# Kernel tuning notes

Hardware: AMD Instinct MI355X
Metric: run time of the kernel (lower is better)

Reference implementation:

```python
import jax, jax.numpy as jnp
import numpy as np

EPS = 1e-8
NEG_INF = -9e15  # matches torch masked_fill value


def setup_inputs() -> dict:
    key = jax.random.key(0)
    k1, k2 = jax.random.split(key)
    B, D = 4096, 512
    p1 = jax.random.normal(k1, (B, D), dtype=jnp.float32)
    p2 = jax.random.normal(k2, (B, D), dtype=jnp.float32)
    return {"p1": p1, "p2": p2}


def reference(p1, p2):
    # NT-Xent / InfoNCE loss as in SimCLR_MODEL.contrastive_loss (temperature = 1).
    z = jnp.concatenate([p1, p2], axis=0)              # [N, D], N = 2B
    # cosine similarity == GEMM of L2-normalized rows (torch eps clamp = 1e-8)
    zn = z / jnp.maximum(jnp.linalg.norm(z, axis=-1, keepdims=True), EPS)
    sim = zn @ zn.T                                     # [N, N]
    N = sim.shape[0]
    idx = jnp.arange(N)
    sim = sim.at[idx, idx].set(NEG_INF)                 # mask self-similarity
    # positive pair of row i is row (i + N/2) mod N (eye rolled by N/2)
    pos = sim[idx, (idx + N // 2) % N]                  # [N]
    nll = -pos + jax.nn.logsumexp(sim, axis=-1)
    return jnp.mean(nll)
```

## Files before the change

### kernel.cpp

```cpp
#include <hip/hip_runtime.h>
#include <hip/hip_bf16.h>
#include <math.h>

#define N_TOT 8192
#define HALF_N 4096
#define D_DIM 512
#define BM 256
#define BK 64
#define NKIT (D_DIM / BK)
#define NTILES 528
#define THREADS 512

typedef float f32x4_t __attribute__((ext_vector_type(4)));
typedef long long i64x2 __attribute__((ext_vector_type(2)));

typedef __attribute__((address_space(1))) unsigned int g_u32;
typedef __attribute__((address_space(3))) unsigned int l_u32;

__global__ __launch_bounds__(256) void k_normalize(
    const float* __restrict__ p1, const float* __restrict__ p2,
    unsigned char* __restrict__ zf8, float* __restrict__ rowsum,
    float* __restrict__ out)
{
    const int w = threadIdx.x >> 6;
    const int lane = threadIdx.x & 63;
    const int row = blockIdx.x * 4 + w;

    if (threadIdx.x < 4) rowsum[blockIdx.x * 4 + threadIdx.x] = 0.0f;
    if (blockIdx.x == 0 && threadIdx.x == 0) out[0] = 0.0f;

    const float* src = (row < HALF_N) ? p1 + (size_t)row * D_DIM
                                      : p2 + (size_t)(row - HALF_N) * D_DIM;
    float4 a = *(const float4*)(src + lane * 4);
    float4 b = *(const float4*)(src + 256 + lane * 4);
    float s = a.x*a.x + a.y*a.y + a.z*a.z + a.w*a.w
            + b.x*b.x + b.y*b.y + b.z*b.z + b.w*b.w;
    #pragma unroll
    for (int m = 1; m < 64; m <<= 1) s += __shfl_xor(s, m, 64);
    float inv = 1.0f / fmaxf(sqrtf(s), 1e-8f);

    int pk0 = __builtin_amdgcn_cvt_pk_fp8_f32(a.x * inv, a.y * inv, 0, false);
    pk0     = __builtin_amdgcn_cvt_pk_fp8_f32(a.z * inv, a.w * inv, pk0, true);
    int pk1 = __builtin_amdgcn_cvt_pk_fp8_f32(b.x * inv, b.y * inv, 0, false);
    pk1     = __builtin_amdgcn_cvt_pk_fp8_f32(b.z * inv, b.w * inv, pk1, true);

    unsigned char* dst = zf8 + (size_t)row * D_DIM;
    const int o0 = lane * 4;
    const int o1 = 256 + lane * 4;
    const int d0 = (o0 & ~63) + ((o0 >> 3) & 3) * 16 + ((o0 >> 5) & 1) * 8 + (o0 & 4);
    const int d1 = (o1 & ~63) + ((o1 >> 3) & 3) * 16 + ((o1 >> 5) & 1) * 8 + (o1 & 4);
    *(int*)(dst + d0) = pk0;
    *(int*)(dst + d1) = pk1;
}

__global__ __launch_bounds__(THREADS, 2) void k_gemm(
    const unsigned char* __restrict__ zf8,
    float* __restrict__ rowsum, float* __restrict__ pos)
{
    __shared__ __align__(16) unsigned char As[2][BM * BK];
    __shared__ __align__(16) unsigned char Bs[2][BM * BK];

    const int tid = threadIdx.x;
    const int lane = tid & 63;
    const int w = tid >> 6;
    const int wr = w >> 2, wc = w & 3;
    const int q = lane >> 4, l15 = lane & 15;

    const int t0 = blockIdx.x;
    const int t = (t0 & 7) * (NTILES / 8) + (t0 >> 3);

    int bi = (int)((sqrtf(8.0f * (float)t + 1.0f) - 1.0f) * 0.5f);
    while ((bi + 1) * (bi + 2) / 2 <= t) ++bi;
    while (bi * (bi + 1) / 2 > t) --bi;
    const int bx = bi;
    const int by = t - bi * (bi + 1) / 2;
    const bool isDiag = (bx == by);
    const bool hasPos = (bx - by == (HALF_N / BM));
    const int rowBase = by * BM;
    const int colBase = bx * BM;

    const int ci0 = tid;
    const int ci1 = tid + THREADS;
    const int r0 = ci0 >> 2, cc0 = ci0 & 3;
    const int r1 = ci1 >> 2, cc1 = ci1 & 3;
    const int gc0 = cc0 ^ ((r0 >> 1) & 3);
    const int gc1 = cc1 ^ ((r1 >> 1) & 3);

    const unsigned char* gA0 = zf8 + (size_t)(rowBase + r0) * D_DIM + gc0 * 16;
    const unsigned char* gA1 = zf8 + (size_t)(rowBase + r1) * D_DIM + gc1 * 16;
    const unsigned char* gB0 = zf8 + (size_t)(colBase + r0) * D_DIM + gc0 * 16;
    const unsigned char* gB1 = zf8 + (size_t)(colBase + r1) * D_DIM + gc1 * 16;

    auto stage = [&](int buf, int kblk) {
        const int kb = kblk * BK;
        __builtin_amdgcn_global_load_lds((const g_u32*)(gA0 + kb), (l_u32*)&As[buf][ci0 * 16], 16, 0, 0);
        __builtin_amdgcn_global_load_lds((const g_u32*)(gA1 + kb), (l_u32*)&As[buf][ci1 * 16], 16, 0, 0);
        __builtin_amdgcn_global_load_lds((const g_u32*)(gB0 + kb), (l_u32*)&Bs[buf][ci0 * 16], 16, 0, 0);
        __builtin_amdgcn_global_load_lds((const g_u32*)(gB1 + kb), (l_u32*)&Bs[buf][ci1 * 16], 16, 0, 0);
    };

    f32x4_t acc[8][4] = {};

    stage(0, 0);

    #pragma unroll
    for (int it = 0; it < NKIT; it++) {
        const int cur = it & 1;
        __syncthreads();
        if (it + 1 < NKIT) stage(cur ^ 1, it + 1);

        i64x2 aF[8], bF[4];
        #pragma unroll
        for (int i = 0; i < 8; i++) {
            const int ra = wr * 128 + i * 16 + l15;
            aF[i] = *(const i64x2*)&As[cur][ra * BK + (q ^ ((ra >> 1) & 3)) * 16];
        }
        #pragma unroll
        for (int j = 0; j < 4; j++) {
            const int rb = wc * 64 + j * 16 + l15;
            bF[j] = *(const i64x2*)&Bs[cur][rb * BK + (q ^ ((rb >> 1) & 3)) * 16];
        }
        #pragma unroll
        for (int h = 0; h < 2; h++)
            #pragma unroll
            for (int i = 0; i < 8; i++)
                #pragma unroll
                for (int j = 0; j < 4; j++)
                    acc[i][j] = __builtin_amdgcn_mfma_f32_16x16x32_fp8_fp8(
                        aF[i][h], bF[j][h], acc[i][j], 0, 0, 0);
    }

    float colacc[4] = {0.f, 0.f, 0.f, 0.f};
    #pragma unroll
    for (int i = 0; i < 8; i++) {
        #pragma unroll
        for (int r = 0; r < 4; r++) {
            const int row = rowBase + wr * 128 + i * 16 + q * 4 + r;
            float rs = 0.0f;
            #pragma unroll
            for (int j = 0; j < 4; j++) {
                const int col = colBase + wc * 64 + j * 16 + l15;
                const float c = acc[i][j][r];
                float e = __expf(c);
                if (isDiag && col == row) e = 0.0f;
                rs += e;
                colacc[j] += e;
                if (hasPos && col == row + HALF_N) { pos[row] = c; pos[col] = c; }
            }
            rs += __shfl_xor(rs, 1); rs += __shfl_xor(rs, 2);
            rs += __shfl_xor(rs, 4); rs += __shfl_xor(rs, 8);
            if (l15 == 0) atomicAdd(&rowsum[row], rs);
        }
    }
    if (!isDiag) {
        #pragma unroll
        for (int j = 0; j < 4; j++) {
            float cs = colacc[j];
            cs += __shfl_xor(cs, 16);
            cs += __shfl_xor(cs, 32);
            if (q == 0) atomicAdd(&rowsum[colBase + wc * 64 + j * 16 + l15], cs);
        }
    }
}

__global__ __launch_bounds__(256) void k_finalize(
    const float* __restrict__ rowsum, const float* __restrict__ pos,
    float* __restrict__ out)
{
    const int t = threadIdx.x;
    const int i = blockIdx.x * 256 + t;
    float s = logf(rowsum[i]) - pos[i];
    #pragma unroll
    for (int m = 1; m < 64; m <<= 1) s += __shfl_xor(s, m, 64);
    __shared__ float red[4];
    if ((t & 63) == 0) red[t >> 6] = s;
    __syncthreads();
    if (t == 0)
        atomicAdd(out, (red[0] + red[1] + red[2] + red[3]) * (1.0f / (float)N_TOT));
}

extern "C" void kernel_launch(void* const* d_in, const int* in_sizes, int n_in,
                              void* d_out, int out_size, void* d_ws, size_t ws_size,
                              hipStream_t stream) {
    const float* p1 = (const float*)d_in[0];
    const float* p2 = (const float*)d_in[1];

    unsigned char* zf8 = (unsigned char*)d_ws;
    float* rowsum = (float*)((char*)d_ws + (size_t)N_TOT * D_DIM);
    float* pos    = rowsum + N_TOT;
    float* outp   = (float*)d_out;

    k_normalize<<<N_TOT / 4, 256, 0, stream>>>(p1, p2, zf8, rowsum, outp);
    k_gemm<<<NTILES, THREADS, 0, stream>>>(zf8, rowsum, pos);
    k_finalize<<<N_TOT / 256, 256, 0, stream>>>(rowsum, pos, outp);
}
```

Baseline: 123.8 us.

## Deepen GEMM to four-stage LDS pipeline with interleaved loads and MFMA phases

Replaces the double-buffered GEMM main loop with a four-slot LDS ring, prefetching three K-blocks ahead. Each iteration is split into four MFMA quadrants, with LDS fragment reads and one async global-to-LDS load interleaved before each. Explicit vmcnt waits, workgroup barriers and s_setprio bracket the MFMA bursts. The aim is to hide global latency and overlap LDS traffic with matrix math. The cost is doubling LDS per block to 128 KB, which likely drops residency to one block per CU and worsens tail behaviour for 528 tiles, plus many extra barriers.

```diff
diff --git a/kernel.cpp b/kernel.cpp
--- a/kernel.cpp
+++ b/kernel.cpp
@@ -11,6 +11,10 @@
 #define NTILES 528
 #define THREADS 512
 
+#define WAIT_VM8 0xF78
+#define WAIT_VM4 0xF74
+#define WAIT_VM0 0xF70
+
 typedef float f32x4_t __attribute__((ext_vector_type(4)));
 typedef long long i64x2 __attribute__((ext_vector_type(2)));
 
@@ -57,8 +61,8 @@
     const unsigned char* __restrict__ zf8,
     float* __restrict__ rowsum, float* __restrict__ pos)
 {
-    __shared__ __align__(16) unsigned char As[2][BM * BK];
-    __shared__ __align__(16) unsigned char Bs[2][BM * BK];
+    __shared__ __align__(16) unsigned char As[4][BM * BK];
+    __shared__ __align__(16) unsigned char Bs[4][BM * BK];
 
     const int tid = threadIdx.x;
     const int lane = tid & 63;
@@ -91,7 +95,7 @@
     const unsigned char* gB0 = zf8 + (size_t)(colBase + r0) * D_DIM + gc0 * 16;
     const unsigned char* gB1 = zf8 + (size_t)(colBase + r1) * D_DIM + gc1 * 16;
 
-    auto stage = [&](int buf, int kblk) {
+    auto stageAll = [&](int buf, int kblk) {
         const int kb = kblk * BK;
         __builtin_amdgcn_global_load_lds((const g_u32*)(gA0 + kb), (l_u32*)&As[buf][ci0 * 16], 16, 0, 0);
         __builtin_amdgcn_global_load_lds((const g_u32*)(gA1 + kb), (l_u32*)&As[buf][ci1 * 16], 16, 0, 0);
@@ -101,34 +105,72 @@
 
     f32x4_t acc[8][4] = {};
 
-    stage(0, 0);
+#define READ_A(i) do { const int ra_ = wr * 128 + (i) * 16 + l15; \
+        aF[i] = *(const i64x2*)&As[cur][ra_ * BK + (q ^ ((ra_ >> 1) & 3)) * 16]; } while (0)
+#define READ_B(j) do { const int rb_ = wc * 64 + (j) * 16 + l15; \
+        bF[j] = *(const i64x2*)&Bs[cur][rb_ * BK + (q ^ ((rb_ >> 1) & 3)) * 16]; } while (0)
+#define QUAD(ih, jh) do { \
+        __builtin_amdgcn_s_setprio(1); \
+        _Pragma("unroll") for (int h_ = 0; h_ < 2; h_++) \
+        _Pragma("unroll") for (int i_ = 0; i_ < 4; i_++) \
+        _Pragma("unroll") for (int j_ = 0; j_ < 2; j_++) \
+            acc[(ih) * 4 + i_][(jh) * 2 + j_] = __builtin_amdgcn_mfma_f32_16x16x32_fp8_fp8( \
+                aF[(ih) * 4 + i_][h_], bF[(jh) * 2 + j_][h_], acc[(ih) * 4 + i_][(jh) * 2 + j_], 0, 0, 0); \
+        __builtin_amdgcn_s_setprio(0); } while (0)
+
+    stageAll(0, 0);
+    stageAll(1, 1);
+    stageAll(2, 2);
+    __builtin_amdgcn_s_waitcnt(WAIT_VM8);
+    __builtin_amdgcn_s_barrier();
+    __builtin_amdgcn_sched_barrier(0);
 
     #pragma unroll
     for (int it = 0; it < NKIT; it++) {
-        const int cur = it & 1;
-        __syncthreads();
-        if (it + 1 < NKIT) stage(cur ^ 1, it + 1);
+        const int cur = it & 3;
+        const int nslot = (it + 3) & 3;
+        const bool doStage = (it + 3) < NKIT;
+        const int kb = (it + 3) * BK;
 
         i64x2 aF[8], bF[4];
-        #pragma unroll
-        for (int i = 0; i < 8; i++) {
-            const int ra = wr * 128 + i * 16 + l15;
-            aF[i] = *(const i64x2*)&As[cur][ra * BK + (q ^ ((ra >> 1) & 3)) * 16];
+
+        READ_A(0); READ_A(1); READ_A(2); READ_A(3);
+        READ_B(0); READ_B(1);
+        if (doStage)
+            __builtin_amdgcn_global_load_lds((const g_u32*)(gA0 + kb), (l_u32*)&As[nslot][ci0 * 16], 16, 0, 0);
+        __builtin_amdgcn_s_barrier();
+        QUAD(0, 0);
+        __builtin_amdgcn_s_barrier();
+
+        READ_B(2); READ_B(3);
+        if (doStage)
+            __builtin_amdgcn_global_load_lds((const g_u32*)(gA1 + kb), (l_u32*)&As[nslot][ci1 * 16], 16, 0, 0);
+        __builtin_amdgcn_s_barrier();
+        QUAD(0, 1);
+        __builtin_amdgcn_s_barrier();
+
+        READ_A(4); READ_A(5); READ_A(6); READ_A(7);
+        if (doStage)
+            __builtin_amdgcn_global_load_lds((const g_u32*)(gB0 + kb), (l_u32*)&Bs[nslot][ci0 * 16], 16, 0, 0);
+        __builtin_amdgcn_s_barrier();
+        QUAD(1, 0);
+        __builtin_amdgcn_s_barrier();
+
+        if (doStage)
+            __builtin_amdgcn_global_load_lds((const g_u32*)(gB1 + kb), (l_u32*)&Bs[nslot][ci1 * 16], 16, 0, 0);
+        __builtin_amdgcn_s_barrier();
+        QUAD(1, 1);
+        if (it < NKIT - 1) {
+            if (it < 5)       __builtin_amdgcn_s_waitcnt(WAIT_VM8);
+            else if (it == 5) __builtin_amdgcn_s_waitcnt(WAIT_VM4);
+            else              __builtin_amdgcn_s_waitcnt(WAIT_VM0);
+            __builtin_amdgcn_s_barrier();
+            __builtin_amdgcn_sched_barrier(0);
         }
-        #pragma unroll
-        for (int j = 0; j < 4; j++) {
-            const int rb = wc * 64 + j * 16 + l15;
-            bF[j] = *(const i64x2*)&Bs[cur][rb * BK + (q ^ ((rb >> 1) & 3)) * 16];
-        }
-        #pragma unroll
-        for (int h = 0; h < 2; h++)
-            #pragma unroll
-            for (int i = 0; i < 8; i++)
-                #pragma unroll
-                for (int j = 0; j < 4; j++)
-                    acc[i][j] = __builtin_amdgcn_mfma_f32_16x16x32_fp8_fp8(
-                        aF[i][h], bF[j][h], acc[i][j], 0, 0, 0);
     }
+#undef READ_A
+#undef READ_B
+#undef QUAD
 
     float colacc[4] = {0.f, 0.f, 0.f, 0.f};
     #pragma unroll
```

Measured after the change: 123.3 us. About the same (-0.4%).
